# Kernel optimization log

Hardware: AMD Instinct MI355X
Metric: run time of the kernel (lower is better)

Reference implementation:

```python
import jax, jax.numpy as jnp
import numpy as np

VOCAB, EMB_DIM, HIDDEN, NUM_CLASSES = 100000, 128, 256, 20
B, S = 4096, 200


def setup_inputs() -> dict:
    key = jax.random.key(0)
    k1, k2, k3, k4, k5, k6, k7 = jax.random.split(key, 7)
    x = jax.random.randint(k1, (B, S), 0, VOCAB, dtype=jnp.int64)
    seq_lengths = jnp.maximum(jax.random.randint(k2, (B,), 0, S, dtype=jnp.int64), 1)
    emb = jax.random.normal(k3, (VOCAB, EMB_DIM), dtype=jnp.float32) * 0.02
    emb = emb.at[0].set(0.0)  # padding_idx=0
    W1 = jax.random.normal(k4, (EMB_DIM, HIDDEN), dtype=jnp.float32) * (1.0 / np.sqrt(EMB_DIM))
    b1 = jax.random.normal(k5, (HIDDEN,), dtype=jnp.float32) * 0.01
    W2 = jax.random.normal(k6, (HIDDEN, NUM_CLASSES), dtype=jnp.float32) * (1.0 / np.sqrt(HIDDEN))
    b2 = jax.random.normal(k7, (NUM_CLASSES,), dtype=jnp.float32) * 0.01
    return {"x": x, "seq_lengths": seq_lengths, "emb": emb, "W1": W1, "b1": b1, "W2": W2, "b2": b2}


def reference(x, seq_lengths, emb, W1, b1, W2, b2):
    # Embedding lookup: [B, S, D]
    e = emb[x]
    # Masked mean over first seq_lengths[i] positions (fused, no per-sample loop)
    mask = (jnp.arange(S)[None, :] < seq_lengths[:, None]).astype(e.dtype)  # [B, S]
    pooled = jnp.einsum('bsd,bs->bd', e, mask) / seq_lengths[:, None].astype(e.dtype)
    # MLP (dropout is identity in eval mode)
    hidden = jax.nn.relu(pooled @ W1 + b1)
    return hidden @ W2 + b2
```

## Files before the change

### kernel.cpp

```cpp
#include <hip/hip_runtime.h>
#include <hip/hip_bf16.h>

#define B 4096
#define S 200
#define EMB_DIM 128
#define HIDDEN 256
#define NUM_CLASSES 20
#define VOCAB 100000
#define RB 2

typedef __attribute__((ext_vector_type(8))) unsigned short ushort8;

__device__ __forceinline__ unsigned short f2bf(float f) {
    unsigned u = __float_as_uint(f);
    unsigned r = u + 0x7fffu + ((u >> 16) & 1u);
    return (unsigned short)(r >> 16);
}

__global__ __launch_bounds__(256) void convert_kernel(
    const float* __restrict__ emb,
    unsigned short* __restrict__ embh)
{
    const long i = ((long)blockIdx.x * 256 + threadIdx.x) * 8;
    const float4 a = *(const float4*)(emb + i);
    const float4 b = *(const float4*)(emb + i + 4);
    ushort8 o;
    o[0] = f2bf(a.x); o[1] = f2bf(a.y); o[2] = f2bf(a.z); o[3] = f2bf(a.w);
    o[4] = f2bf(b.x); o[5] = f2bf(b.y); o[6] = f2bf(b.z); o[7] = f2bf(b.w);
    *(ushort8*)(embh + i) = o;
}

__global__ __launch_bounds__(256) void fused_kernel(
    const int* __restrict__ x,
    const int* __restrict__ lens,
    const unsigned short* __restrict__ embh,
    const float* __restrict__ W1,
    const float* __restrict__ b1,
    const float* __restrict__ W2,
    const float* __restrict__ b2,
    float* __restrict__ out)
{
    __shared__ int   sidx[RB][256];
    __shared__ float tmp[16][16][8];
    __shared__ float P[RB][EMB_DIM];
    __shared__ float H[RB][HIDDEN];
    __shared__ float part[RB][4][NUM_CLASSES];

    const int t  = threadIdx.x;
    const int b0 = blockIdx.x * RB;

    int Ls[RB];
    #pragma unroll
    for (int r = 0; r < RB; ++r) {
        Ls[r] = lens[b0 + r];
        int v = 0;
        if (t < Ls[r]) v = x[(long)(b0 + r) * S + t];
        sidx[r][t] = v;
    }
    __syncthreads();

    const int g = t >> 4;
    const int d = t & 15;

    for (int r = 0; r < RB; ++r) {
        const int L = Ls[r];
        const int nIter = ((L + 63) & ~63) >> 6;

        float acc[4][8];
        #pragma unroll
        for (int j = 0; j < 4; ++j)
            #pragma unroll
            for (int f = 0; f < 8; ++f) acc[j][f] = 0.f;

        int cur[4], nxt[4];
        #pragma unroll
        for (int j = 0; j < 4; ++j) cur[j] = sidx[r][g + 16 * j];

        for (int it = 0; it < nIter; ++it) {
            uint4 v[4];
            #pragma unroll
            for (int j = 0; j < 4; ++j)
                v[j] = *(const uint4*)(embh + (long)cur[j] * EMB_DIM + d * 8);

            if (it + 1 < nIter) {
                const int nb = (it + 1) << 6;
                #pragma unroll
                for (int j = 0; j < 4; ++j) nxt[j] = sidx[r][nb + g + 16 * j];
            }

            #pragma unroll
            for (int j = 0; j < 4; ++j) {
                const unsigned c0 = v[j].x, c1 = v[j].y, c2 = v[j].z, c3 = v[j].w;
                acc[j][0] += __uint_as_float(c0 << 16);
                acc[j][1] += __uint_as_float(c0 & 0xffff0000u);
                acc[j][2] += __uint_as_float(c1 << 16);
                acc[j][3] += __uint_as_float(c1 & 0xffff0000u);
                acc[j][4] += __uint_as_float(c2 << 16);
                acc[j][5] += __uint_as_float(c2 & 0xffff0000u);
                acc[j][6] += __uint_as_float(c3 << 16);
                acc[j][7] += __uint_as_float(c3 & 0xffff0000u);
            }
            #pragma unroll
            for (int j = 0; j < 4; ++j) cur[j] = nxt[j];
        }

        #pragma unroll
        for (int f = 0; f < 8; ++f)
            tmp[g][d][f] = acc[0][f] + acc[1][f] + acc[2][f] + acc[3][f];
        __syncthreads();

        if (t < EMB_DIM) {
            float s = 0.f;
            #pragma unroll
            for (int gg = 0; gg < 16; ++gg) s += tmp[gg][t >> 3][t & 7];
            P[r][t] = s / (float)L;
        }
        __syncthreads();
    }

    {
        float h0a = 0.f, h0b = 0.f, h1a = 0.f, h1b = 0.f;
        for (int k = 0; k < EMB_DIM; k += 2) {
            const float wa = W1[(k)     * HIDDEN + t];
            const float wb = W1[(k + 1) * HIDDEN + t];
            h0a += P[0][k] * wa;  h0b += P[0][k + 1] * wb;
            h1a += P[1][k] * wa;  h1b += P[1][k + 1] * wb;
        }
        const float bb = b1[t];
        H[0][t] = fmaxf(h0a + h0b + bb, 0.f);
        H[1][t] = fmaxf(h1a + h1b + bb, 0.f);
    }
    __syncthreads();

    if (t < RB * 4 * NUM_CLASSES) {
        const int r  = t / (4 * NUM_CLASSES);
        const int u  = t - r * 4 * NUM_CLASSES;
        const int j  = u / NUM_CLASSES;
        const int c  = u - j * NUM_CLASSES;
        const int k0 = j * 64;
        float a = 0.f;
        for (int k = k0; k < k0 + 64; ++k)
            a += H[r][k] * W2[k * NUM_CLASSES + c];
        part[r][j][c] = a;
    }
    __syncthreads();

    if (t < RB * NUM_CLASSES) {
        const int r = t / NUM_CLASSES;
        const int c = t - r * NUM_CLASSES;
        const float a = b2[c] + part[r][0][c] + part[r][1][c]
                              + part[r][2][c] + part[r][3][c];
        out[(long)(b0 + r) * NUM_CLASSES + c] = a;
    }
}

extern "C" void kernel_launch(void* const* d_in, const int* in_sizes, int n_in,
                              void* d_out, int out_size, void* d_ws, size_t ws_size,
                              hipStream_t stream) {
    const int*   x    = (const int*)d_in[0];
    const int*   lens = (const int*)d_in[1];
    const float* emb  = (const float*)d_in[2];
    const float* W1   = (const float*)d_in[3];
    const float* b1   = (const float*)d_in[4];
    const float* W2   = (const float*)d_in[5];
    const float* b2   = (const float*)d_in[6];
    float*       out  = (float*)d_out;

    unsigned short* embh = (unsigned short*)d_ws;

    convert_kernel<<<(VOCAB * EMB_DIM) / (8 * 256), 256, 0, stream>>>(emb, embh);
    fused_kernel<<<B / RB, 256, 0, stream>>>(x, lens, embh, W1, b1, W2, b2, out);
}
```

Before: 125.0 us.

## Assign one wavefront per sample and process eight samples per block

The fused kernel now uses 512 threads and eight rows per block, with each 64-lane wavefront pooling one sample independently. Before, all 256 threads worked on each row in turn with block-wide syncs between rows. The cross-group reduction now uses wave shuffles instead of shared memory and barriers. The MLP stage reuses each W1 load across four rows instead of two. Per-wave loop trip counts follow each sample's own length, which reduces wasted 64-token padding, but warps within a block now have unbalanced lengths and the larger block may lower occupancy.

```diff
diff --git a/kernel.cpp b/kernel.cpp
--- a/kernel.cpp
+++ b/kernel.cpp
@@ -7,7 +7,9 @@
 #define HIDDEN 256
 #define NUM_CLASSES 20
 #define VOCAB 100000
-#define RB 2
+#define RB 8
+#define NT (RB * 64)
+#define SP 208
 
 typedef __attribute__((ext_vector_type(8))) unsigned short ushort8;
 
@@ -30,7 +32,7 @@
     *(ushort8*)(embh + i) = o;
 }
 
-__global__ __launch_bounds__(256) void fused_kernel(
+__global__ __launch_bounds__(NT) void fused_kernel(
     const int* __restrict__ x,
     const int* __restrict__ lens,
     const unsigned short* __restrict__ embh,
@@ -40,117 +42,120 @@
     const float* __restrict__ b2,
     float* __restrict__ out)
 {
-    __shared__ int   sidx[RB][256];
-    __shared__ float tmp[16][16][8];
+    __shared__ int   sidx[RB][SP];
     __shared__ float P[RB][EMB_DIM];
     __shared__ float H[RB][HIDDEN];
-    __shared__ float part[RB][4][NUM_CLASSES];
 
-    const int t  = threadIdx.x;
-    const int b0 = blockIdx.x * RB;
+    const int t    = threadIdx.x;
+    const int w    = t >> 6;
+    const int lane = t & 63;
+    const int b0   = blockIdx.x * RB;
+    const int row  = b0 + w;
+    const int L    = lens[row];
 
-    int Ls[RB];
-    #pragma unroll
-    for (int r = 0; r < RB; ++r) {
-        Ls[r] = lens[b0 + r];
+    for (int p = lane; p < SP; p += 64) {
         int v = 0;
-        if (t < Ls[r]) v = x[(long)(b0 + r) * S + t];
-        sidx[r][t] = v;
+        if (p < L) v = x[(long)row * S + p];
+        sidx[w][p] = v;
     }
     __syncthreads();
 
-    const int g = t >> 4;
-    const int d = t & 15;
+    const int g = lane >> 4;
+    const int d = lane & 15;
 
-    for (int r = 0; r < RB; ++r) {
-        const int L = Ls[r];
-        const int nIter = ((L + 63) & ~63) >> 6;
+    const int nR = (L + 15) >> 4;
 
-        float acc[4][8];
+    float acc[4][8];
+    #pragma unroll
+    for (int j = 0; j < 4; ++j)
+        #pragma unroll
+        for (int f = 0; f < 8; ++f) acc[j][f] = 0.f;
+
+    int cur[4], nxt[4];
+    #pragma unroll
+    for (int j = 0; j < 4; ++j) cur[j] = sidx[w][g + 4 * j];
+
+    for (int it = 0; it < nR; ++it) {
+        uint4 v[4];
         #pragma unroll
         for (int j = 0; j < 4; ++j)
+            v[j] = *(const uint4*)(embh + (long)cur[j] * EMB_DIM + d * 8);
+
+        if (it + 1 < nR) {
+            const int base = (it + 1) << 4;
             #pragma unroll
-            for (int f = 0; f < 8; ++f) acc[j][f] = 0.f;
-
-        int cur[4], nxt[4];
-        #pragma unroll
-        for (int j = 0; j < 4; ++j) cur[j] = sidx[r][g + 16 * j];
-
-        for (int it = 0; it < nIter; ++it) {
-            uint4 v[4];
-            #pragma unroll
-            for (int j = 0; j < 4; ++j)
-                v[j] = *(const uint4*)(embh + (long)cur[j] * EMB_DIM + d * 8);
-
-            if (it + 1 < nIter) {
-                const int nb = (it + 1) << 6;
-                #pragma unroll
-                for (int j = 0; j < 4; ++j) nxt[j] = sidx[r][nb + g + 16 * j];
-            }
-
-            #pragma unroll
-            for (int j = 0; j < 4; ++j) {
-                const unsigned c0 = v[j].x, c1 = v[j].y, c2 = v[j].z, c3 = v[j].w;
-                acc[j][0] += __uint_as_float(c0 << 16);
-                acc[j][1] += __uint_as_float(c0 & 0xffff0000u);
-                acc[j][2] += __uint_as_float(c1 << 16);
-                acc[j][3] += __uint_as_float(c1 & 0xffff0000u);
-                acc[j][4] += __uint_as_float(c2 << 16);
-                acc[j][5] += __uint_as_float(c2 & 0xffff0000u);
-                acc[j][6] += __uint_as_float(c3 << 16);
-                acc[j][7] += __uint_as_float(c3 & 0xffff0000u);
-            }
-            #pragma unroll
-            for (int j = 0; j < 4; ++j) cur[j] = nxt[j];
+            for (int j = 0; j < 4; ++j) nxt[j] = sidx[w][base + g + 4 * j];
         }
 
         #pragma unroll
-        for (int f = 0; f < 8; ++f)
-            tmp[g][d][f] = acc[0][f] + acc[1][f] + acc[2][f] + acc[3][f];
-        __syncthreads();
-
-        if (t < EMB_DIM) {
-            float s = 0.f;
-            #pragma unroll
-            for (int gg = 0; gg < 16; ++gg) s += tmp[gg][t >> 3][t & 7];
-            P[r][t] = s / (float)L;
+        for (int j = 0; j < 4; ++j) {
+            const unsigned c0 = v[j].x, c1 = v[j].y, c2 = v[j].z, c3 = v[j].w;
+            acc[j][0] += __uint_as_float(c0 << 16);
+            acc[j][1] += __uint_as_float(c0 & 0xffff0000u);
+            acc[j][2] += __uint_as_float(c1 << 16);
+            acc[j][3] += __uint_as_float(c1 & 0xffff0000u);
+            acc[j][4] += __uint_as_float(c2 << 16);
+            acc[j][5] += __uint_as_float(c2 & 0xffff0000u);
+            acc[j][6] += __uint_as_float(c3 << 16);
+            acc[j][7] += __uint_as_float(c3 & 0xffff0000u);
         }
-        __syncthreads();
+        #pragma unroll
+        for (int j = 0; j < 4; ++j) cur[j] = nxt[j];
     }
 
-    {
-        float h0a = 0.f, h0b = 0.f, h1a = 0.f, h1b = 0.f;
-        for (int k = 0; k < EMB_DIM; k += 2) {
-            const float wa = W1[(k)     * HIDDEN + t];
-            const float wb = W1[(k + 1) * HIDDEN + t];
-            h0a += P[0][k] * wa;  h0b += P[0][k + 1] * wb;
-            h1a += P[1][k] * wa;  h1b += P[1][k + 1] * wb;
-        }
-        const float bb = b1[t];
-        H[0][t] = fmaxf(h0a + h0b + bb, 0.f);
-        H[1][t] = fmaxf(h1a + h1b + bb, 0.f);
+    float v8[8];
+    #pragma unroll
+    for (int f = 0; f < 8; ++f) {
+        float s = acc[0][f] + acc[1][f] + acc[2][f] + acc[3][f];
+        s += __shfl_down(s, 32);
+        s += __shfl_down(s, 16);
+        v8[f] = s;
+    }
+    if (lane < 16) {
+        const float invL = 1.0f / (float)L;
+        float4 q0 = make_float4(v8[0] * invL, v8[1] * invL, v8[2] * invL, v8[3] * invL);
+        float4 q1 = make_float4(v8[4] * invL, v8[5] * invL, v8[6] * invL, v8[7] * invL);
+        *(float4*)&P[w][8 * lane]     = q0;
+        *(float4*)&P[w][8 * lane + 4] = q1;
     }
     __syncthreads();
 
-    if (t < RB * 4 * NUM_CLASSES) {
-        const int r  = t / (4 * NUM_CLASSES);
-        const int u  = t - r * 4 * NUM_CLASSES;
-        const int j  = u / NUM_CLASSES;
-        const int c  = u - j * NUM_CLASSES;
-        const int k0 = j * 64;
-        float a = 0.f;
-        for (int k = k0; k < k0 + 64; ++k)
-            a += H[r][k] * W2[k * NUM_CLASSES + c];
-        part[r][j][c] = a;
+    {
+        const int h  = t & 255;
+        const int r0 = (t >> 8) * 4;
+        float a0 = 0.f, a1 = 0.f, a2 = 0.f, a3 = 0.f;
+        for (int k4 = 0; k4 < EMB_DIM; k4 += 4) {
+            const float4 p0 = *(const float4*)&P[r0 + 0][k4];
+            const float4 p1 = *(const float4*)&P[r0 + 1][k4];
+            const float4 p2 = *(const float4*)&P[r0 + 2][k4];
+            const float4 p3 = *(const float4*)&P[r0 + 3][k4];
+            #pragma unroll
+            for (int kk = 0; kk < 4; ++kk) {
+                const float wv = W1[(k4 + kk) * HIDDEN + h];
+                const float e0 = (kk == 0) ? p0.x : (kk == 1) ? p0.y : (kk == 2) ? p0.z : p0.w;
+                const float e1 = (kk == 0) ? p1.x : (kk == 1) ? p1.y : (kk == 2) ? p1.z : p1.w;
+                const float e2 = (kk == 0) ? p2.x : (kk == 1) ? p2.y : (kk == 2) ? p2.z : p2.w;
+                const float e3 = (kk == 0) ? p3.x : (kk == 1) ? p3.y : (kk == 2) ? p3.z : p3.w;
+                a0 += e0 * wv; a1 += e1 * wv; a2 += e2 * wv; a3 += e3 * wv;
+            }
+        }
+        const float bb = b1[h];
+        H[r0 + 0][h] = fmaxf(a0 + bb, 0.f);
+        H[r0 + 1][h] = fmaxf(a1 + bb, 0.f);
+        H[r0 + 2][h] = fmaxf(a2 + bb, 0.f);
+        H[r0 + 3][h] = fmaxf(a3 + bb, 0.f);
     }
     __syncthreads();
 
-    if (t < RB * NUM_CLASSES) {
-        const int r = t / NUM_CLASSES;
-        const int c = t - r * NUM_CLASSES;
-        const float a = b2[c] + part[r][0][c] + part[r][1][c]
-                              + part[r][2][c] + part[r][3][c];
-        out[(long)(b0 + r) * NUM_CLASSES + c] = a;
+    if (lane < NUM_CLASSES) {
+        const int r = w;
+        const int c = lane;
+        float a0 = 0.f, a1 = 0.f;
+        for (int k = 0; k < HIDDEN; k += 2) {
+            a0 += H[r][k]     * W2[(k)     * NUM_CLASSES + c];
+            a1 += H[r][k + 1] * W2[(k + 1) * NUM_CLASSES + c];
+        }
+        out[(long)(b0 + r) * NUM_CLASSES + c] = a0 + a1 + b2[c];
     }
 }
 
@@ -169,5 +174,5 @@
     unsigned short* embh = (unsigned short*)d_ws;
 
     convert_kernel<<<(VOCAB * EMB_DIM) / (8 * 256), 256, 0, stream>>>(emb, embh);
-    fused_kernel<<<B / RB, 256, 0, stream>>>(x, lens, embh, W1, b1, W2, b2, out);
+    fused_kernel<<<B / RB, NT, 0, stream>>>(x, lens, embh, W1, b1, W2, b2, out);
 }
```

Result: slower. 128.6 us (+2.8%).
